# Kernel optimization log

Hardware: AMD Instinct MI355X
Metric: run time of the kernel (lower is better)

## Reference

```python
import jax, jax.numpy as jnp
import numpy as np

N_SRC = 50000
N_DST = 50000
E = 640000
D = 128


def setup_inputs() -> dict:
    key = jax.random.key(0)
    k1, k2, k3, k4 = jax.random.split(key, 4)
    src_feat = jax.random.normal(k1, (N_SRC, D), dtype=jnp.float32)
    dst_feat = jax.random.normal(k2, (N_DST, D), dtype=jnp.float32)
    # nn.Linear(2*D, 1): weight [1, 2D] -> stored transposed [2D, 1], bias [1]
    att_w = jax.random.normal(k3, (2 * D, 1), dtype=jnp.float32) / np.sqrt(2 * D)
    att_b = jnp.zeros((1,), dtype=jnp.float32)
    edge_index = jax.random.randint(k4, (2, E), 0, N_DST, dtype=jnp.int64)
    return {
        "src_feat": src_feat,
        "dst_feat": dst_feat,
        "att_w": att_w,
        "att_b": att_b,
        "edge_index": edge_index,
        "n_dst": N_DST,
    }


def reference(src_feat, dst_feat, att_w, att_b, edge_index, n_dst):
    src_idx = edge_index[0]
    dst_idx = edge_index[1]
    src_sel = src_feat[src_idx]  # [E, D] gather
    dst_sel = dst_feat[dst_idx]  # [E, D] gather
    # Linear on concat([src, dst]) == src @ w_src + dst @ w_dst + b (avoids materializing [E, 2D])
    d = src_feat.shape[1]
    logits = src_sel @ att_w[:d] + dst_sel @ att_w[d:] + att_b  # [E, 1]
    att = jax.nn.sigmoid(logits)  # [E, 1]
    weighted = src_sel * att  # [E, D]
    agg = jax.ops.segment_sum(weighted, dst_idx, num_segments=n_dst)  # [n_dst, D]
    count = jax.ops.segment_sum(att, dst_idx, num_segments=n_dst)  # [n_dst, 1]
    count = jnp.maximum(count, 1e-8)
    return agg / count
```

## Files before the change

### kernel.cpp

```cpp
#include <hip/hip_runtime.h>
#include <hip/hip_fp16.h>
#include <math.h>

#define D 128
#define CAP 64

struct __align__(8) half4 { __half2 a, b; };

__global__ void prep_dots_kernel(const float* __restrict__ src_feat,
                                 const float* __restrict__ dst_feat,
                                 const float* __restrict__ w,
                                 const float* __restrict__ bias,
                                 float* __restrict__ ssum,
                                 float* __restrict__ dsum,
                                 unsigned short* __restrict__ src16,
                                 int* __restrict__ cnt,
                                 int n_src, int n_total, int n_dst) {
    int gid = blockIdx.x * blockDim.x + threadIdx.x;
    if (gid < n_dst) cnt[gid] = 0;
    int wv    = gid >> 6;
    int lane  = threadIdx.x & 63;
    int node  = wv * 2 + (lane >> 5);
    int q     = lane & 31;
    if (node >= n_total) return;
    const float* row;
    const float* wp;
    float b = 0.0f;
    if (node < n_src) { row = src_feat + (size_t)node * D; wp = w; }
    else { row = dst_feat + (size_t)(node - n_src) * D; wp = w + D; b = bias[0]; }
    float4 r  = ((const float4*)row)[q];
    float4 w4 = ((const float4*)wp)[q];
    if (node < n_src) {
        half4 h;
        h.a = __floats2half2_rn(r.x, r.y);
        h.b = __floats2half2_rn(r.z, r.w);
        ((half4*)(src16 + (size_t)node * D))[q] = h;
    }
    float v = r.x * w4.x + r.y * w4.y + r.z * w4.z + r.w * w4.w;
    #pragma unroll
    for (int off = 16; off > 0; off >>= 1) v += __shfl_xor(v, off, 64);
    if (q == 0) {
        if (node < n_src) ssum[node] = v;
        else              dsum[node - n_src] = v + b;
    }
}

__global__ void fill_kernel(const int* __restrict__ src_idx,
                            const int* __restrict__ dst_idx,
                            int* __restrict__ cnt,
                            unsigned short* __restrict__ bucket, int E) {
    int i = (blockIdx.x * blockDim.x + threadIdx.x) * 4;
    if (i + 4 <= E) {
        int4 s4 = *(const int4*)(src_idx + i);
        int4 d4 = *(const int4*)(dst_idx + i);
        int p0 = atomicAdd(&cnt[d4.x], 1);
        int p1 = atomicAdd(&cnt[d4.y], 1);
        int p2 = atomicAdd(&cnt[d4.z], 1);
        int p3 = atomicAdd(&cnt[d4.w], 1);
        if (p0 < CAP) bucket[(size_t)d4.x * CAP + p0] = (unsigned short)s4.x;
        if (p1 < CAP) bucket[(size_t)d4.y * CAP + p1] = (unsigned short)s4.y;
        if (p2 < CAP) bucket[(size_t)d4.z * CAP + p2] = (unsigned short)s4.z;
        if (p3 < CAP) bucket[(size_t)d4.w * CAP + p3] = (unsigned short)s4.w;
    } else {
        for (int j = i; j < E; j++) {
            int s = src_idx[j];
            int d = dst_idx[j];
            int pos = atomicAdd(&cnt[d], 1);
            if (pos < CAP) bucket[(size_t)d * CAP + pos] = (unsigned short)s;
        }
    }
}

__global__ void gather_kernel(const unsigned short* __restrict__ src16,
                              const float* __restrict__ ssum,
                              const float* __restrict__ dsum,
                              const int* __restrict__ cnt,
                              const unsigned short* __restrict__ bucket,
                              float* __restrict__ out, int n_dst) {
    int d = (blockIdx.x * blockDim.x + threadIdx.x) >> 6;
    if (d >= n_dst) return;
    int lane = threadIdx.x & 63;
    int half = lane >> 5;
    int q    = lane & 31;
    int len = min(cnt[d], CAP);
    float dsv = dsum[d];
    int   sv = 0;
    float av = 0.f;
    if (lane < len) {
        sv = (int)bucket[(size_t)d * CAP + lane];
        av = 1.0f / (1.0f + expf(-(ssum[sv] + dsv)));
    }
    float4 acc = make_float4(0.f, 0.f, 0.f, 0.f);
    float asum = 0.f;
    int j = 0;
    for (; j + 8 <= len; j += 8) {
        int e0 = j + half, e1 = j + 2 + half, e2 = j + 4 + half, e3 = j + 6 + half;
        int   s0 = __shfl(sv, e0, 64);
        int   s1 = __shfl(sv, e1, 64);
        int   s2 = __shfl(sv, e2, 64);
        int   s3 = __shfl(sv, e3, 64);
        float a0 = __shfl(av, e0, 64);
        float a1 = __shfl(av, e1, 64);
        float a2 = __shfl(av, e2, 64);
        float a3 = __shfl(av, e3, 64);
        half4 h0 = ((const half4*)(src16 + (size_t)s0 * D))[q];
        half4 h1 = ((const half4*)(src16 + (size_t)s1 * D))[q];
        half4 h2 = ((const half4*)(src16 + (size_t)s2 * D))[q];
        half4 h3 = ((const half4*)(src16 + (size_t)s3 * D))[q];
        float2 f0a = __half22float2(h0.a), f0b = __half22float2(h0.b);
        float2 f1a = __half22float2(h1.a), f1b = __half22float2(h1.b);
        float2 f2a = __half22float2(h2.a), f2b = __half22float2(h2.b);
        float2 f3a = __half22float2(h3.a), f3b = __half22float2(h3.b);
        acc.x += a0 * f0a.x + a1 * f1a.x + a2 * f2a.x + a3 * f3a.x;
        acc.y += a0 * f0a.y + a1 * f1a.y + a2 * f2a.y + a3 * f3a.y;
        acc.z += a0 * f0b.x + a1 * f1b.x + a2 * f2b.x + a3 * f3b.x;
        acc.w += a0 * f0b.y + a1 * f1b.y + a2 * f2b.y + a3 * f3b.y;
        asum += a0 + a1 + a2 + a3;
    }
    for (; j < len; j += 2) {
        int e0 = j + half;
        int   s0 = __shfl(sv, e0, 64);
        float a0 = __shfl(av, e0, 64);
        half4 h0 = ((const half4*)(src16 + (size_t)s0 * D))[q];
        float2 f0a = __half22float2(h0.a), f0b = __half22float2(h0.b);
        acc.x += a0 * f0a.x;
        acc.y += a0 * f0a.y;
        acc.z += a0 * f0b.x;
        acc.w += a0 * f0b.y;
        asum += a0;
    }
    acc.x += __shfl_xor(acc.x, 32, 64);
    acc.y += __shfl_xor(acc.y, 32, 64);
    acc.z += __shfl_xor(acc.z, 32, 64);
    acc.w += __shfl_xor(acc.w, 32, 64);
    asum  += __shfl_xor(asum,  32, 64);
    float inv = 1.0f / fmaxf(asum, 1e-8f);
    if (half == 0) {
        float4* orow = (float4*)(out + (size_t)d * D);
        orow[q] = make_float4(acc.x * inv, acc.y * inv, acc.z * inv, acc.w * inv);
    }
}

extern "C" void kernel_launch(void* const* d_in, const int* in_sizes, int n_in,
                              void* d_out, int out_size, void* d_ws, size_t ws_size,
                              hipStream_t stream) {
    const float* src_feat = (const float*)d_in[0];
    const float* dst_feat = (const float*)d_in[1];
    const float* att_w    = (const float*)d_in[2];
    const float* att_b    = (const float*)d_in[3];
    const int*   edges    = (const int*)d_in[4];

    const int d     = in_sizes[2] / 2;
    const int n_src = in_sizes[0] / d;
    const int n_dst = in_sizes[1] / d;
    const int E     = in_sizes[4] / 2;

    const int* src_idx = edges;
    const int* dst_idx = edges + E;

    float* out = (float*)d_out;

    char* ws = (char*)d_ws;
    unsigned short* src16  = (unsigned short*)ws; ws += sizeof(unsigned short) * (size_t)n_src * D;
    unsigned short* bucket = (unsigned short*)ws; ws += sizeof(unsigned short) * (size_t)n_dst * CAP;
    float* ssum = (float*)ws;                     ws += sizeof(float) * n_src;
    float* dsum = (float*)ws;                     ws += sizeof(float) * n_dst;
    int*   cnt  = (int*)ws;                       ws += sizeof(int) * n_dst;

    {
        int n_total = n_src + n_dst;
        int n_waves = (n_total + 1) / 2;
        long long threads_total = (long long)n_waves * 64;
        int blocks = (int)((threads_total + 255) / 256);
        prep_dots_kernel<<<blocks, 256, 0, stream>>>(src_feat, dst_feat, att_w, att_b,
                                                     ssum, dsum, src16, cnt,
                                                     n_src, n_total, n_dst);
    }
    {
        int nthreads = (E + 3) / 4;
        fill_kernel<<<(nthreads + 255) / 256, 256, 0, stream>>>(src_idx, dst_idx,
                                                                cnt, bucket, E);
    }
    {
        long long threads_total = (long long)n_dst * 64;
        int blocks = (int)((threads_total + 255) / 256);
        gather_kernel<<<blocks, 256, 0, stream>>>(src16, ssum, dsum, cnt, bucket,
                                                  out, n_dst);
    }
}
```

Before: 164.8 us.

## Fuse dots and bucket fill into one kernel with destination-partitioned fill

Merges the per-node dot/fp16-conversion kernel and the edge bucket-fill kernel into one launch, with the first block range doing fill work and the rest doing dots, so the two phases can overlap. The fill now splits destinations into 8 partitions; each group of blocks scans all edges and only handles destinations in its partition. The aim is better atomic locality in cache. The cost is that dst_idx is read 8 times and the counter zeroing moves to its own small kernel launch.

```diff
diff --git a/kernel.cpp b/kernel.cpp
--- a/kernel.cpp
+++ b/kernel.cpp
@@ -4,69 +4,93 @@
 
 #define D 128
 #define CAP 64
+#define NPART 8
+#define FILL_BLOCKS 1024
 
 struct __align__(8) half4 { __half2 a, b; };
 
-__global__ void prep_dots_kernel(const float* __restrict__ src_feat,
+__global__ void zero_cnt_kernel(int* __restrict__ cnt, int n) {
+    int i = blockIdx.x * blockDim.x + threadIdx.x;
+    if (i < n) cnt[i] = 0;
+}
+
+__global__ void dots_fill_kernel(const float* __restrict__ src_feat,
                                  const float* __restrict__ dst_feat,
                                  const float* __restrict__ w,
                                  const float* __restrict__ bias,
+                                 const int* __restrict__ src_idx,
+                                 const int* __restrict__ dst_idx,
                                  float* __restrict__ ssum,
                                  float* __restrict__ dsum,
                                  unsigned short* __restrict__ src16,
                                  int* __restrict__ cnt,
-                                 int n_src, int n_total, int n_dst) {
-    int gid = blockIdx.x * blockDim.x + threadIdx.x;
-    if (gid < n_dst) cnt[gid] = 0;
-    int wv    = gid >> 6;
-    int lane  = threadIdx.x & 63;
-    int node  = wv * 2 + (lane >> 5);
-    int q     = lane & 31;
-    if (node >= n_total) return;
-    const float* row;
-    const float* wp;
-    float b = 0.0f;
-    if (node < n_src) { row = src_feat + (size_t)node * D; wp = w; }
-    else { row = dst_feat + (size_t)(node - n_src) * D; wp = w + D; b = bias[0]; }
-    float4 r  = ((const float4*)row)[q];
-    float4 w4 = ((const float4*)wp)[q];
-    if (node < n_src) {
-        half4 h;
-        h.a = __floats2half2_rn(r.x, r.y);
-        h.b = __floats2half2_rn(r.z, r.w);
-        ((half4*)(src16 + (size_t)node * D))[q] = h;
-    }
-    float v = r.x * w4.x + r.y * w4.y + r.z * w4.z + r.w * w4.w;
-    #pragma unroll
-    for (int off = 16; off > 0; off >>= 1) v += __shfl_xor(v, off, 64);
-    if (q == 0) {
-        if (node < n_src) ssum[node] = v;
-        else              dsum[node - n_src] = v + b;
-    }
-}
-
-__global__ void fill_kernel(const int* __restrict__ src_idx,
-                            const int* __restrict__ dst_idx,
-                            int* __restrict__ cnt,
-                            unsigned short* __restrict__ bucket, int E) {
-    int i = (blockIdx.x * blockDim.x + threadIdx.x) * 4;
-    if (i + 4 <= E) {
-        int4 s4 = *(const int4*)(src_idx + i);
-        int4 d4 = *(const int4*)(dst_idx + i);
-        int p0 = atomicAdd(&cnt[d4.x], 1);
-        int p1 = atomicAdd(&cnt[d4.y], 1);
-        int p2 = atomicAdd(&cnt[d4.z], 1);
-        int p3 = atomicAdd(&cnt[d4.w], 1);
-        if (p0 < CAP) bucket[(size_t)d4.x * CAP + p0] = (unsigned short)s4.x;
-        if (p1 < CAP) bucket[(size_t)d4.y * CAP + p1] = (unsigned short)s4.y;
-        if (p2 < CAP) bucket[(size_t)d4.z * CAP + p2] = (unsigned short)s4.z;
-        if (p3 < CAP) bucket[(size_t)d4.w * CAP + p3] = (unsigned short)s4.w;
+                                 unsigned short* __restrict__ bucket,
+                                 int E, int n_src, int n_total, int n_dst) {
+    if (blockIdx.x < FILL_BLOCKS) {
+        const int p    = blockIdx.x & (NPART - 1);
+        const int bsub = blockIdx.x >> 3;
+        const int nsub = FILL_BLOCKS / NPART;
+        const int part = (n_dst + NPART - 1) / NPART;
+        const int lo = p * part;
+        const int hi = min(lo + part, n_dst);
+        const int nchunks = (E + 3) / 4;
+        int tid    = bsub * blockDim.x + threadIdx.x;
+        int stride = nsub * blockDim.x;
+        for (int c = tid; c < nchunks; c += stride) {
+            int base = c * 4;
+            if (base + 4 <= E) {
+                int4 d4 = *(const int4*)(dst_idx + base);
+                if (d4.x >= lo && d4.x < hi) {
+                    int pos = atomicAdd(&cnt[d4.x], 1);
+                    if (pos < CAP) bucket[(size_t)d4.x * CAP + pos] = (unsigned short)src_idx[base];
+                }
+                if (d4.y >= lo && d4.y < hi) {
+                    int pos = atomicAdd(&cnt[d4.y], 1);
+                    if (pos < CAP) bucket[(size_t)d4.y * CAP + pos] = (unsigned short)src_idx[base + 1];
+                }
+                if (d4.z >= lo && d4.z < hi) {
+                    int pos = atomicAdd(&cnt[d4.z], 1);
+                    if (pos < CAP) bucket[(size_t)d4.z * CAP + pos] = (unsigned short)src_idx[base + 2];
+                }
+                if (d4.w >= lo && d4.w < hi) {
+                    int pos = atomicAdd(&cnt[d4.w], 1);
+                    if (pos < CAP) bucket[(size_t)d4.w * CAP + pos] = (unsigned short)src_idx[base + 3];
+                }
+            } else {
+                for (int j = base; j < E; j++) {
+                    int dd = dst_idx[j];
+                    if (dd >= lo && dd < hi) {
+                        int pos = atomicAdd(&cnt[dd], 1);
+                        if (pos < CAP) bucket[(size_t)dd * CAP + pos] = (unsigned short)src_idx[j];
+                    }
+                }
+            }
+        }
     } else {
-        for (int j = i; j < E; j++) {
-            int s = src_idx[j];
-            int d = dst_idx[j];
-            int pos = atomicAdd(&cnt[d], 1);
-            if (pos < CAP) bucket[(size_t)d * CAP + pos] = (unsigned short)s;
+        int wv   = (blockIdx.x - FILL_BLOCKS) * (blockDim.x >> 6) + (threadIdx.x >> 6);
+        int lane = threadIdx.x & 63;
+        int node = wv * 2 + (lane >> 5);
+        int q    = lane & 31;
+        if (node >= n_total) return;
+        const float* row;
+        const float* wp;
+        float b = 0.0f;
+        if (node < n_src) { row = src_feat + (size_t)node * D; wp = w; }
+        else { row = dst_feat + (size_t)(node - n_src) * D; wp = w + D; b = bias[0]; }
+        float4 r  = ((const float4*)row)[q];
+        float4 w4 = ((const float4*)wp)[q];
+        if (node < n_src) {
+            half4 h;
+            h.a = __floats2half2_rn(r.x, r.y);
+            h.b = __floats2half2_rn(r.z, r.w);
+            ((half4*)(src16 + (size_t)node * D))[q] = h;
+        }
+        float v = r.x * w4.x + r.y * w4.y + r.z * w4.z + r.w * w4.w;
+        #pragma unroll
+        for (int off = 16; off > 0; off >>= 1) v += __shfl_xor(v, off, 64);
+        if (q == 0) {
+            if (node < n_src) ssum[node] = v;
+            else              dsum[node - n_src] = v + b;
         }
     }
 }
@@ -167,20 +191,19 @@
     float* dsum = (float*)ws;                     ws += sizeof(float) * n_dst;
     int*   cnt  = (int*)ws;                       ws += sizeof(int) * n_dst;
 
+    zero_cnt_kernel<<<(n_dst + 255) / 256, 256, 0, stream>>>(cnt, n_dst);
+
     {
         int n_total = n_src + n_dst;
         int n_waves = (n_total + 1) / 2;
-        long long threads_total = (long long)n_waves * 64;
-        int blocks = (int)((threads_total + 255) / 256);
-        prep_dots_kernel<<<blocks, 256, 0, stream>>>(src_feat, dst_feat, att_w, att_b,
-                                                     ssum, dsum, src16, cnt,
-                                                     n_src, n_total, n_dst);
-    }
-    {
-        int nthreads = (E + 3) / 4;
-        fill_kernel<<<(nthreads + 255) / 256, 256, 0, stream>>>(src_idx, dst_idx,
-                                                                cnt, bucket, E);
-    }
+        int dots_blocks = (n_waves + 3) / 4;
+        int blocks = FILL_BLOCKS + dots_blocks;
+        dots_fill_kernel<<<blocks, 256, 0, stream>>>(src_feat, dst_feat, att_w, att_b,
+                                                     src_idx, dst_idx, ssum, dsum,
+                                                     src16, cnt, bucket,
+                                                     E, n_src, n_total, n_dst);
+    }
+
     {
         long long threads_total = (long long)n_dst * 64;
         int blocks = (int)((threads_total + 255) / 256);
```

After: 152.1 us. -7.7%, faster.
